# Kernel optimization log

Measured on AMD Instinct MI355X. Metric: run time of the kernel, lower is better.

## Reference

```python
import jax, jax.numpy as jnp
import numpy as np
import math

HEADS = 16
DIMS = 1024
SEQ_LEN = 2048
RANK_K = 128
BATCH = 8


def setup_inputs() -> dict:
    key = jax.random.key(0)
    ks = jax.random.split(key, 14)
    dh_std = 1.0 / math.sqrt(DIMS)
    proj_std = 1.0 / math.sqrt(RANK_K)
    inp = {
        "q": jax.random.normal(ks[0], (BATCH, SEQ_LEN, DIMS), jnp.float32),
        "k": jax.random.normal(ks[1], (BATCH, SEQ_LEN, DIMS), jnp.float32),
        "v": jax.random.normal(ks[2], (BATCH, SEQ_LEN, DIMS), jnp.float32),
        # nn.Linear weights [out, in], bias [out]
        "Wq": jax.random.uniform(ks[3], (DIMS, DIMS), jnp.float32, -dh_std, dh_std),
        "bq": jax.random.uniform(ks[4], (DIMS,), jnp.float32, -dh_std, dh_std),
        "Wk": jax.random.uniform(ks[5], (DIMS, DIMS), jnp.float32, -dh_std, dh_std),
        "bk": jax.random.uniform(ks[6], (DIMS,), jnp.float32, -dh_std, dh_std),
        "Wv": jax.random.uniform(ks[7], (DIMS, DIMS), jnp.float32, -dh_std, dh_std),
        "bv": jax.random.uniform(ks[8], (DIMS,), jnp.float32, -dh_std, dh_std),
        # Linformer low-rank projections [seq_length, k], uniform(-1/sqrt(k), 1/sqrt(k))
        "proj_k": jax.random.uniform(ks[9], (SEQ_LEN, RANK_K), jnp.float32, -proj_std, proj_std),
        "proj_v": jax.random.uniform(ks[10], (SEQ_LEN, RANK_K), jnp.float32, -proj_std, proj_std),
        "Wo": jax.random.uniform(ks[11], (DIMS, DIMS), jnp.float32, -dh_std, dh_std),
        "bo": jax.random.uniform(ks[12], (DIMS,), jnp.float32, -dh_std, dh_std),
    }
    return inp


def reference(q, k, v, Wq, bq, Wk, bk, Wv, bv, proj_k, proj_v, Wo, bo):
    B, N, D = q.shape
    H = HEADS
    dh = D // H
    Kr = proj_k.shape[1]

    kp = k @ Wk.T + bk                       # [B, N, D]
    # faithful to original: plain reshape (view), NOT a head-split transpose
    qp = (q @ Wq.T + bq).reshape(B, H, N, dh)  # [B, H, N, dh]
    vp = v @ Wv.T + bv                       # [B, N, D]

    pk = jnp.einsum('bnd,nk->bkd', kp, proj_k[:N])  # [B, Kr, D]
    pv = jnp.einsum('bnd,nk->bkd', vp, proj_v[:N])  # [B, Kr, D]
    pk = pk.reshape(B, Kr, H, dh).transpose(0, 2, 1, 3)  # [B, H, Kr, dh]
    pv = pv.reshape(B, Kr, H, dh).transpose(0, 2, 1, 3)  # [B, H, Kr, dh]

    # scores [B,H,N,Kr] -> transposed to [B,H,Kr,N]; softmax over N (seq) axis
    scores = jnp.einsum('bhnd,bhkd->bhkn', qp, pk) / math.sqrt(dh)
    attn = jax.nn.softmax(scores, axis=-1)   # [B, H, Kr, N]
    out = jnp.einsum('bhkn,bhkd->bhnd', attn, pv)  # [B, H, N, dh]
    out = out.transpose(0, 2, 1, 3).reshape(B, N, D)
    return out @ Wo.T + bo
```

## Files before the change

### kernel.cpp

```cpp
#include <hip/hip_runtime.h>

typedef unsigned short u16;
typedef unsigned int   u32;
typedef __attribute__((ext_vector_type(4))) float fx4;
typedef __attribute__((ext_vector_type(8))) __bf16 bf16x8;
typedef __attribute__((ext_vector_type(8))) unsigned short us8;
typedef __attribute__((ext_vector_type(2))) unsigned int u32x2;

__device__ __forceinline__ u16 f2bf(float x){
  u32 u = __builtin_bit_cast(u32, x);
  u += 0x7fffu + ((u >> 16) & 1u);
  return (u16)(u >> 16);
}
__device__ __forceinline__ float b2f(u16 h){
  u32 u = ((u32)h) << 16;
  return __builtin_bit_cast(float, u);
}
__device__ __forceinline__ void gld16(const void* g, void* l){
  __builtin_amdgcn_global_load_lds(
      (const __attribute__((address_space(1))) u32*)g,
      (__attribute__((address_space(3))) u32*)l, 16, 0, 0);
}
__device__ __forceinline__ void xcd_remap(u32& bx, u32& by, u32& bz){
  u32 nx = gridDim.x, ny = gridDim.y, nz = gridDim.z;
  u32 nwg = nx * ny * nz;
  u32 orig = (blockIdx.z * ny + blockIdx.y) * nx + blockIdx.x;
  u32 lid = (orig & 7u) * (nwg >> 3) + (orig >> 3);
  bx = lid % nx;
  u32 rem = lid / nx;
  by = rem % ny;
  bz = rem / ny;
}

__global__ __launch_bounds__(256) void k_f2bfAll(const float* __restrict__ w0,
                                                 const float* __restrict__ w1,
                                                 const float* __restrict__ w2,
                                                 const float* __restrict__ w3,
                                                 const float* __restrict__ q,
                                                 u16* __restrict__ wout,
                                                 u16* __restrict__ qout,
                                                 float* __restrict__ zbuf){
  if (blockIdx.x == 0 && blockIdx.y == 0) zbuf[threadIdx.x] = 0.f;
  const int y = blockIdx.y;
  const float* src;
  u16* dst;
  if (y < 4){
    src = y == 0 ? w0 : y == 1 ? w1 : y == 2 ? w2 : w3;
    dst = wout + (long)y * 1048576;
  } else {
    src = q + (long)(y - 4) * 1048576;
    dst = qout + (long)(y - 4) * 1048576;
  }
  int i = blockIdx.x * 256 + threadIdx.x;
  const int stride = gridDim.x * 256;
  for (; i < 131072; i += stride){
    const float4* p = (const float4*)src + (long)i * 2;
    float4 a = p[0], b = p[1];
    us8 o = { f2bf(a.x), f2bf(a.y), f2bf(a.z), f2bf(a.w),
              f2bf(b.x), f2bf(b.y), f2bf(b.z), f2bf(b.w) };
    *((us8*)dst + i) = o;
  }
}

__global__ __launch_bounds__(256) void k_tconvKV(const float* __restrict__ ksrc,
                                                 const float* __restrict__ vsrc,
                                                 u16* __restrict__ kT){
  const int z = blockIdx.z;
  const float* in = (z >= 8 ? vsrc : ksrc) + (long)(z & 7) * 2097152;
  u16* out = kT + (long)(z >> 3) * 16777216 + (long)(z & 7) * 2097152;
  const int c0 = blockIdx.x * 64, r0 = blockIdx.y * 64;
  const int t = threadIdx.x;
  const int c4 = t & 15, r4 = t >> 4;
  float4 f[4];
  #pragma unroll
  for (int i = 0; i < 4; ++i)
    f[i] = *(const float4*)(in + (long)(r0 + r4 * 4 + i) * 1024 + c0 + c4 * 4);
  #pragma unroll
  for (int j = 0; j < 4; ++j){
    u32 lo = (u32)f2bf(((const float*)&f[0])[j]) | ((u32)f2bf(((const float*)&f[1])[j]) << 16);
    u32 hi = (u32)f2bf(((const float*)&f[2])[j]) | ((u32)f2bf(((const float*)&f[3])[j]) << 16);
    u32x2 pr = { lo, hi };
    *(u32x2*)(out + (long)(c0 + c4 * 4 + j) * 2048 + r0 + r4 * 4) = pr;
  }
}

__global__ __launch_bounds__(256) void k_tconvP(const float* __restrict__ pjk,
                                                const float* __restrict__ pjv,
                                                u16* __restrict__ projT,
                                                float* __restrict__ ssum){
  const int z = blockIdx.z;
  const float* in = z ? pjv : pjk;
  u16* out = projT + z * 262144;
  float* colsum = ssum + z * 128;
  const int c0 = blockIdx.x * 64, r0 = blockIdx.y * 64;
  __shared__ u16 tile[64][66];
  __shared__ float red[256];
  const int t = threadIdx.x;
  const int cc = t & 63, wq = t >> 6;
  float part = 0.f;
  #pragma unroll
  for (int i = 0; i < 16; ++i){
    int rr = i * 4 + wq;
    float v = in[(long)(r0 + rr) * 128 + c0 + cc];
    tile[rr][cc] = f2bf(v);
    part += v;
  }
  red[t] = part;
  __syncthreads();
  if (t < 64){
    float s = red[t] + red[t + 64] + red[t + 128] + red[t + 192];
    atomicAdd(&colsum[c0 + t], s);
  }
  __syncthreads();
  const int oc0 = t >> 5, jb = (t & 31) * 2;
  #pragma unroll
  for (int i = 0; i < 8; ++i){
    int oc = oc0 + i * 8;
    u32 pk2 = (u32)tile[jb][oc] | ((u32)tile[jb + 1][oc] << 16);
    *(u32*)(out + (long)(c0 + oc) * 2048 + r0 + jb) = pk2;
  }
}

template<int BM, int BN, int MODE, int EPI, typename OutT>
__global__ __launch_bounds__(256) void k_gemm(
    const u16* __restrict__ A, int lda, long sAz,
    const u16* __restrict__ B, int ldb, long sBz,
    OutT* __restrict__ C, int ldc, long sCz,
    int K, const float* __restrict__ bias, const float* __restrict__ srow, float scale)
{
  constexpr int BK = 64;
  constexpr int FM = BM / 32, FN = BN / 32;
  __shared__ u16 ldsA[BM * BK];
  __shared__ u16 ldsB[BN * BK];
  u32 bx, by, bz;
  xcd_remap(bx, by, bz);
  const long z = bz;
  if constexpr (MODE == 0){ A += z * sAz; B += z * sBz; C += z * sCz; }
  if constexpr (MODE == 3){ long p = z >> 3, bb = z & 7;
                            A += p * 262144; B += p * 16777216 + bb * 2097152;
                            C += p * 1048576 + bb * 131072; }
  const int t = threadIdx.x;
  const int lane = t & 63;
  const int w = t >> 6, wm = w >> 1, wn = w & 1;
  const int r15 = lane & 15, g = lane >> 4;
  const int m0 = by * BM, n0 = bx * BN;
  fx4 acc[FM][FN] = {};
  constexpr int CA = BM * BK / (8 * 256);
  constexpr int CB = BN * BK / (8 * 256);
  for (int kt = 0; kt < K; kt += BK){
    #pragma unroll
    for (int i = 0; i < CA; ++i){
      int ch = i * 256 + t, row = ch >> 3, cc = ch & 7;
      gld16(A + (long)(m0 + row) * lda + kt + cc * 8, (char*)ldsA + ch * 16);
    }
    #pragma unroll
    for (int i = 0; i < CB; ++i){
      int ch = i * 256 + t, row = ch >> 3, cc = ch & 7;
      gld16(B + (long)(n0 + row) * ldb + kt + cc * 8, (char*)ldsB + ch * 16);
    }
    __syncthreads();
    #pragma unroll
    for (int ks = 0; ks < 2; ++ks){
      bf16x8 af[FM], bfv[FN];
      #pragma unroll
      for (int mf = 0; mf < FM; ++mf)
        af[mf] = *(const bf16x8*)&ldsA[(wm * (BM/2) + mf * 16 + r15) * BK + ks * 32 + g * 8];
      #pragma unroll
      for (int nf = 0; nf < FN; ++nf)
        bfv[nf] = *(const bf16x8*)&ldsB[(wn * (BN/2) + nf * 16 + r15) * BK + ks * 32 + g * 8];
      #pragma unroll
      for (int mf = 0; mf < FM; ++mf)
        #pragma unroll
        for (int nf = 0; nf < FN; ++nf)
          acc[mf][nf] = __builtin_amdgcn_mfma_f32_16x16x32_bf16(af[mf], bfv[nf], acc[mf][nf], 0, 0, 0);
    }
    __syncthreads();
  }
  #pragma unroll
  for (int mf = 0; mf < FM; ++mf){
    #pragma unroll
    for (int nf = 0; nf < FN; ++nf){
      const int row0 = m0 + wm * (BM/2) + mf * 16 + g * 4;
      const int col  = n0 + wn * (BN/2) + nf * 16 + r15;
      float vv[4];
      #pragma unroll
      for (int r = 0; r < 4; ++r){
        float v = acc[mf][nf][r];
        if constexpr (EPI == 1) v += bias[col];
        vv[r] = v;
      }
      #pragma unroll
      for (int r = 0; r < 4; ++r){
        if constexpr (sizeof(OutT) == 2) C[(long)(row0 + r) * ldc + col] = (OutT)f2bf(vv[r]);
        else                             C[(long)(row0 + r) * ldc + col] = (OutT)vv[r];
      }
    }
  }
}

__global__ __launch_bounds__(256) void k_pkpv(
    const u16* __restrict__ ck, const u16* __restrict__ Wk_bf,
    const u16* __restrict__ Wv_bf, const float* __restrict__ bk,
    const float* __restrict__ bv, const float* __restrict__ ssum,
    u16* __restrict__ pk, u16* __restrict__ pvT)
{
  constexpr int BM = 64, BN = 64, BK = 64;
  __shared__ u16 ldsA[BM * BK];
  __shared__ u16 ldsB[BN * BK];
  u32 bx, by, bz;
  xcd_remap(bx, by, bz);
  const int half = bz >> 3, b = bz & 7;
  const u16* A = ck + half * 1048576 + b * 131072;
  const u16* B = half ? Wv_bf : Wk_bf;
  const float* bias = half ? bv : bk;
  const float* srow = ssum + half * 128;
  const float scale = half ? 1.f : 0.125f;
  const int t = threadIdx.x;
  const int lane = t & 63;
  const int w = t >> 6, wm = w >> 1, wn = w & 1;
  const int r15 = lane & 15, g = lane >> 4;
  const int m0 = by * BM, n0 = bx * BN;
  fx4 acc[2][2] = {};
  for (int kt = 0; kt < 1024; kt += BK){
    #pragma unroll
    for (int i = 0; i < 2; ++i){
      int ch = i * 256 + t, row = ch >> 3, cc = ch & 7;
      gld16(A + (long)(m0 + row) * 1024 + kt + cc * 8, (char*)ldsA + ch * 16);
    }
    #pragma unroll
    for (int i = 0; i < 2; ++i){
      int ch = i * 256 + t, row = ch >> 3, cc = ch & 7;
      gld16(B + (long)(n0 + row) * 1024 + kt + cc * 8, (char*)ldsB + ch * 16);
    }
    __syncthreads();
    #pragma unroll
    for (int ks = 0; ks < 2; ++ks){
      bf16x8 af[2], bfv[2];
      #pragma unroll
      for (int mf = 0; mf < 2; ++mf)
        af[mf] = *(const bf16x8*)&ldsA[(wm * 32 + mf * 16 + r15) * BK + ks * 32 + g * 8];
      #pragma unroll
      for (int nf = 0; nf < 2; ++nf)
        bfv[nf] = *(const bf16x8*)&ldsB[(wn * 32 + nf * 16 + r15) * BK + ks * 32 + g * 8];
      #pragma unroll
      for (int mf = 0; mf < 2; ++mf)
        #pragma unroll
        for (int nf = 0; nf < 2; ++nf)
          acc[mf][nf] = __builtin_amdgcn_mfma_f32_16x16x32_bf16(af[mf], bfv[nf], acc[mf][nf], 0, 0, 0);
    }
    __syncthreads();
  }
  #pragma unroll
  for (int mf = 0; mf < 2; ++mf){
    #pragma unroll
    for (int nf = 0; nf < 2; ++nf){
      const int row0 = m0 + wm * 32 + mf * 16 + g * 4;
      const int col  = n0 + wn * 32 + nf * 16 + r15;
      float vv[4];
      #pragma unroll
      for (int r = 0; r < 4; ++r)
        vv[r] = (acc[mf][nf][r] + srow[row0 + r] * bias[col]) * scale;
      if (!half){
        #pragma unroll
        for (int r = 0; r < 4; ++r)
          pk[b * 131072 + (long)(row0 + r) * 1024 + col] = f2bf(vv[r]);
      } else {
        u32 lo = (u32)f2bf(vv[0]) | ((u32)f2bf(vv[1]) << 16);
        u32 hi = (u32)f2bf(vv[2]) | ((u32)f2bf(vv[3]) << 16);
        u32x2 pk2 = { lo, hi };
        *(u32x2*)(pvT + b * 131072 + (long)col * 128 + row0) = pk2;
      }
    }
  }
}

template<int EPI, typename OutT>
__global__ __launch_bounds__(512, 1) void k_gemm256b(
    const u16* __restrict__ A, int lda,
    const u16* __restrict__ B, int ldb,
    OutT* __restrict__ C, int ldc,
    int K, const float* __restrict__ bias)
{
  constexpr int BM = 256, BN = 256, BK = 64;
  __shared__ u16 ldsA[2][BM * BK];
  __shared__ u16 ldsB[2][BN * BK];
  u32 bx, by, bz;
  xcd_remap(bx, by, bz);
  const int m0 = by * BM, n0 = bx * BN;
  const int t = threadIdx.x, lane = t & 63, w = t >> 6;
  const int wm = w >> 2, wn = w & 3;
  const int r15 = lane & 15, g = lane >> 4;
  const int NT = K >> 6;

  auto stA = [&](int buf, int half, int kt){
    #pragma unroll
    for (int j = 0; j < 2; ++j){
      int ch = j * 512 + t, row = ch >> 3, cc = ch & 7;
      gld16(A + (long)(m0 + half * 128 + row) * lda + kt + ((cc ^ (row & 7)) * 8),
            (char*)ldsA[buf] + half * 16384 + ch * 16);
    }
  };
  auto stB = [&](int buf, int half, int kt){
    #pragma unroll
    for (int j = 0; j < 2; ++j){
      int ch = j * 512 + t, row = ch >> 3, cc = ch & 7;
      gld16(B + (long)(n0 + half * 128 + row) * ldb + kt + ((cc ^ (row & 7)) * 8),
            (char*)ldsB[buf] + half * 16384 + ch * 16);
    }
  };

  stB(0,0,0); stB(0,1,0); stA(0,0,0); stA(0,1,0);
  if (NT > 1){ stB(1,0,BK); stB(1,1,BK); stA(1,0,BK); }
  asm volatile("s_waitcnt vmcnt(6)" ::: "memory");
  __builtin_amdgcn_s_barrier();
  asm volatile("" ::: "memory");

  fx4 acc[8][4] = {};
  for (int tt = 0; tt < NT; ++tt){
    const int buf = tt & 1;
    bf16x8 a[2][4], b01[2][2], b23[2][2];
    #pragma unroll
    for (int ks = 0; ks < 2; ++ks)
      #pragma unroll
      for (int mf = 0; mf < 4; ++mf){
        int row = wm * 128 + mf * 16 + r15;
        a[ks][mf] = *(const bf16x8*)((const char*)ldsA[buf] + row * 128 + (((ks*4+g) ^ (r15 & 7)) * 16));
      }
    #pragma unroll
    for (int ks = 0; ks < 2; ++ks)
      #pragma unroll
      for (int nf = 0; nf < 2; ++nf){
        int row = wn * 64 + nf * 16 + r15;
        b01[ks][nf] = *(const bf16x8*)((const char*)ldsB[buf] + row * 128 + (((ks*4+g) ^ (r15 & 7)) * 16));
      }
    if (tt + 1 < NT) stA(buf ^ 1, 1, (tt + 1) * BK);
    __builtin_amdgcn_s_setprio(1);
    #pragma unroll
    for (int ks = 0; ks < 2; ++ks)
      #pragma unroll
      for (int mf = 0; mf < 4; ++mf)
        #pragma unroll
        for (int nf = 0; nf < 2; ++nf)
          acc[mf][nf] = __builtin_amdgcn_mfma_f32_16x16x32_bf16(a[ks][mf], b01[ks][nf], acc[mf][nf], 0, 0, 0);
    __builtin_amdgcn_s_setprio(0);
    asm volatile("" ::: "memory");
    __builtin_amdgcn_s_barrier();
    asm volatile("" ::: "memory");
    #pragma unroll
    for (int ks = 0; ks < 2; ++ks)
      #pragma unroll
      for (int nf = 0; nf < 2; ++nf){
        int row = wn * 64 + (nf + 2) * 16 + r15;
        b23[ks][nf] = *(const bf16x8*)((const char*)ldsB[buf] + row * 128 + (((ks*4+g) ^ (r15 & 7)) * 16));
      }
    __builtin_amdgcn_s_setprio(1);
    #pragma unroll
    for (int ks = 0; ks < 2; ++ks)
      #pragma unroll
      for (int mf = 0; mf < 4; ++mf)
        #pragma unroll
        for (int nf = 0; nf < 2; ++nf)
          acc[mf][nf + 2] = __builtin_amdgcn_mfma_f32_16x16x32_bf16(a[ks][mf], b23[ks][nf], acc[mf][nf + 2], 0, 0, 0);
    __builtin_amdgcn_s_setprio(0);
    asm volatile("" ::: "memory");
    __builtin_amdgcn_s_barrier();
    asm volatile("" ::: "memory");
    #pragma unroll
    for (int ks = 0; ks < 2; ++ks)
      #pragma unroll
      for (int mf = 0; mf < 4; ++mf){
        int row = wm * 128 + (mf + 4) * 16 + r15;
        a[ks][mf] = *(const bf16x8*)((const char*)ldsA[buf] + row * 128 + (((ks*4+g) ^ (r15 & 7)) * 16));
      }
    if (tt + 2 < NT) stB(buf, 0, (tt + 2) * BK);
    __builtin_amdgcn_s_setprio(1);
    #pragma unroll
    for (int ks = 0; ks < 2; ++ks)
      #pragma unroll
      for (int mf = 0; mf < 4; ++mf)
        #pragma unroll
        for (int nf = 0; nf < 2; ++nf)
          acc[mf + 4][nf + 2] = __builtin_amdgcn_mfma_f32_16x16x32_bf16(a[ks][mf], b23[ks][nf], acc[mf + 4][nf + 2], 0, 0, 0);
    __builtin_amdgcn_s_setprio(0);
    asm volatile("" ::: "memory");
    __builtin_amdgcn_s_barrier();
    asm volatile("" ::: "memory");
    if (tt + 2 < NT){ stA(buf, 0, (tt + 2) * BK); stB(buf, 1, (tt + 2) * BK); }
    __builtin_amdgcn_s_setprio(1);
    #pragma unroll
    for (int ks = 0; ks < 2; ++ks)
      #pragma unroll
      for (int mf = 0; mf < 4; ++mf)
        #pragma unroll
        for (int nf = 0; nf < 2; ++nf)
          acc[mf + 4][nf] = __builtin_amdgcn_mfma_f32_16x16x32_bf16(a[ks][mf], b01[ks][nf], acc[mf + 4][nf], 0, 0, 0);
    __builtin_amdgcn_s_setprio(0);
    if (tt + 2 < NT)      { asm volatile("s_waitcnt vmcnt(6)" ::: "memory"); }
    else if (tt + 1 < NT) { asm volatile("s_waitcnt vmcnt(0)" ::: "memory"); }
    asm volatile("" ::: "memory");
    __builtin_amdgcn_s_barrier();
    asm volatile("" ::: "memory");
  }

  #pragma unroll
  for (int mf = 0; mf < 8; ++mf)
    #pragma unroll
    for (int nf = 0; nf < 4; ++nf){
      const int row0 = m0 + wm * 128 + mf * 16 + g * 4;
      const int col  = n0 + wn * 64 + nf * 16 + r15;
      float bcol = 0.f;
      if constexpr (EPI == 1) bcol = bias[col];
      #pragma unroll
      for (int r = 0; r < 4; ++r){
        float vv = acc[mf][nf][r] + bcol;
        if constexpr (sizeof(OutT) == 2) C[(long)(row0 + r) * ldc + col] = (OutT)f2bf(vv);
        else                             C[(long)(row0 + r) * ldc + col] = (OutT)vv;
      }
    }
}

__global__ __launch_bounds__(512) void k_stats(const u16* __restrict__ pk,
                                               const u16* __restrict__ qp,
                                               float* __restrict__ zpart){
  const int hf = blockIdx.x, z = blockIdx.y;
  const int b = z >> 4, h = z & 15;
  const u16* pkh = pk + b * 131072 + h * 64;
  const u16* qph = qp + (long)z * 131072;
  __shared__ u16 pkL[128 * 64];
  __shared__ float zred[8][128];
  const int t = threadIdx.x, lane = t & 63, w = t >> 6;
  const int r15 = lane & 15, g = lane >> 4;
  #pragma unroll
  for (int i = 0; i < 2; ++i){
    int ch = i * 512 + t, row = ch >> 3, cc = ch & 7;
    int csrc = cc ^ (row & 7);
    gld16(pkh + (long)row * 1024 + csrc * 8, (char*)pkL + ch * 16);
  }
  __syncthreads();
  float zacc[8][4] = {};
  for (int c = 0; c < 4; ++c){
    const int n0 = hf * 1024 + w * 128 + c * 32;
    fx4 acc[8][2] = {};
    #pragma unroll
    for (int ks = 0; ks < 2; ++ks){
      bf16x8 bq[2];
      #pragma unroll
      for (int nf = 0; nf < 2; ++nf)
        bq[nf] = *(const bf16x8*)(qph + (long)(n0 + nf * 16 + r15) * 64 + ks * 32 + g * 8);
      #pragma unroll
      for (int mf = 0; mf < 8; ++mf){
        int row = mf * 16 + r15;
        int x = (ks * 4 + g) ^ (row & 7);
        bf16x8 a = *(const bf16x8*)((const char*)pkL + row * 128 + x * 16);
        #pragma unroll
        for (int nf = 0; nf < 2; ++nf)
          acc[mf][nf] = __builtin_amdgcn_mfma_f32_16x16x32_bf16(a, bq[nf], acc[mf][nf], 0, 0, 0);
      }
    }
    #pragma unroll
    for (int mf = 0; mf < 8; ++mf)
      #pragma unroll
      for (int nf = 0; nf < 2; ++nf)
        #pragma unroll
        for (int r = 0; r < 4; ++r)
          zacc[mf][r] += __expf(acc[mf][nf][r]);
  }
  #pragma unroll
  for (int mf = 0; mf < 8; ++mf)
    #pragma unroll
    for (int r = 0; r < 4; ++r){
      float v = zacc[mf][r];
      v += __shfl_xor(v, 1); v += __shfl_xor(v, 2);
      v += __shfl_xor(v, 4); v += __shfl_xor(v, 8);
      zacc[mf][r] = v;
    }
  if (r15 == 0){
    #pragma unroll
    for (int mf = 0; mf < 8; ++mf)
      #pragma unroll
      for (int r = 0; r < 4; ++r)
        zred[w][mf * 16 + g * 4 + r] = zacc[mf][r];
  }
  __syncthreads();
  if (t < 128){
    float s = 0.f;
    #pragma unroll
    for (int w2 = 0; w2 < 8; ++w2) s += zred[w2][t];
    zpart[hf * 16384 + (long)z * 128 + t] = s;
  }
}

__global__ __launch_bounds__(256) void k_attn(const u16* __restrict__ pk,
                                              const u16* __restrict__ qp,
                                              const u16* __restrict__ pvT,
                                              const float* __restrict__ zpart,
                                              u16* __restrict__ outh){
  u32 bx, by, bz;
  xcd_remap(bx, by, bz);
  const int z = by, nb = bx;
  const int b = z >> 4, h = z & 15;
  const u16* pkh = pk  + b * 131072 + h * 64;
  const u16* qph = qp  + (long)z * 131072;
  const u16* pvh = pvT + b * 131072 + h * 8192;
  __shared__ u16 pkL[128 * 64];
  __shared__ u16 ptL[4][32 * 132];
  __shared__ float zL[128];
  const int t = threadIdx.x, lane = t & 63, w = t >> 6;
  const int r15 = lane & 15, g = lane >> 4;
  #pragma unroll
  for (int i = 0; i < 4; ++i){
    int ch = i * 256 + t, row = ch >> 3, cc = ch & 7;
    int csrc = cc ^ (row & 7);
    gld16(pkh + (long)row * 1024 + csrc * 8, (char*)pkL + ch * 16);
  }
  if (t < 128)
    zL[t] = 1.0f / (zpart[(long)z * 128 + t] + zpart[16384 + (long)z * 128 + t]);
  __syncthreads();
  const int n0 = nb * 128 + w * 32;
  fx4 acc[8][2] = {};
  #pragma unroll
  for (int ks = 0; ks < 2; ++ks){
    bf16x8 bq[2];
    #pragma unroll
    for (int nf = 0; nf < 2; ++nf)
      bq[nf] = *(const bf16x8*)(qph + (long)(n0 + nf * 16 + r15) * 64 + ks * 32 + g * 8);
    #pragma unroll
    for (int mf = 0; mf < 8; ++mf){
      int row = mf * 16 + r15;
      int x = (ks * 4 + g) ^ (row & 7);
      bf16x8 a = *(const bf16x8*)((const char*)pkL + row * 128 + x * 16);
      #pragma unroll
      for (int nf = 0; nf < 2; ++nf)
        acc[mf][nf] = __builtin_amdgcn_mfma_f32_16x16x32_bf16(a, bq[nf], acc[mf][nf], 0, 0, 0);
    }
  }
  u16* pt = ptL[w];
  #pragma unroll
  for (int mf = 0; mf < 8; ++mf){
    const int kb = mf * 16 + g * 4;
    const float z0 = zL[kb], z1 = zL[kb + 1], z2 = zL[kb + 2], z3 = zL[kb + 3];
    #pragma unroll
    for (int nf = 0; nf < 2; ++nf){
      const int nl = nf * 16 + r15;
      u32 lo = (u32)f2bf(__expf(acc[mf][nf][0]) * z0) |
               ((u32)f2bf(__expf(acc[mf][nf][1]) * z1) << 16);
      u32 hi = (u32)f2bf(__expf(acc[mf][nf][2]) * z2) |
               ((u32)f2bf(__expf(acc[mf][nf][3]) * z3) << 16);
      u32x2 pkd = { lo, hi };
      *(u32x2*)(pt + nl * 132 + kb) = pkd;
    }
  }
  fx4 o[2][4] = {};
  #pragma unroll
  for (int ks = 0; ks < 4; ++ks){
    bf16x8 bv[4];
    #pragma unroll
    for (int nf = 0; nf < 4; ++nf)
      bv[nf] = *(const bf16x8*)(pvh + (long)(nf * 16 + r15) * 128 + ks * 32 + g * 8);
    #pragma unroll
    for (int mf = 0; mf < 2; ++mf){
      bf16x8 pa = *(const bf16x8*)(pt + (mf * 16 + r15) * 132 + ks * 32 + g * 8);
      #pragma unroll
      for (int nf = 0; nf < 4; ++nf)
        o[mf][nf] = __builtin_amdgcn_mfma_f32_16x16x32_bf16(pa, bv[nf], o[mf][nf], 0, 0, 0);
    }
  }
  u16* og = outh + ((long)b * 2048 + n0) * 1024 + h * 64;
  #pragma unroll
  for (int mf = 0; mf < 2; ++mf)
    #pragma unroll
    for (int nf = 0; nf < 4; ++nf)
      #pragma unroll
      for (int r = 0; r < 4; ++r){
        int nl = mf * 16 + g * 4 + r;
        og[(long)nl * 1024 + nf * 16 + r15] = f2bf(o[mf][nf][r]);
      }
}

extern "C" void kernel_launch(void* const* d_in, const int* in_sizes, int n_in,
                              void* d_out, int out_size, void* d_ws, size_t ws_size,
                              hipStream_t stream)
{
  const float* q   = (const float*)d_in[0];
  const float* k   = (const float*)d_in[1];
  const float* v   = (const float*)d_in[2];
  const float* Wq  = (const float*)d_in[3];
  const float* bq  = (const float*)d_in[4];
  const float* Wk  = (const float*)d_in[5];
  const float* bk  = (const float*)d_in[6];
  const float* Wv  = (const float*)d_in[7];
  const float* bv  = (const float*)d_in[8];
  const float* pjk = (const float*)d_in[9];
  const float* pjv = (const float*)d_in[10];
  const float* Wo  = (const float*)d_in[11];
  const float* bo  = (const float*)d_in[12];

  if (ws_size < 152044544u) return;

  char* ws = (char*)d_ws;
  u16*  q_bf  = (u16*)(ws + 0);
  u16*  kT    = (u16*)(ws + 33554432);
  u16*  vT    = (u16*)(ws + 67108864);
  u16*  W_bf  = (u16*)(ws + 100663296);
  u16*  projT = (u16*)(ws + 109051904);
  float* sk   = (float*)(ws + 110100480);
  u16*  qp    = (u16*)(ws + 110101504);
  u16*  ck    = (u16*)(ws + 143655936);
  u16*  pk    = (u16*)(ws + 147850240);
  u16*  pvT   = (u16*)(ws + 149947392);
  float* zpart = (float*)(ws + 33554432);
  u16*  outh  = (u16*)(ws + 0);
  u16*  Wq_bf = W_bf, *Wk_bf = W_bf + 1048576, *Wv_bf = W_bf + 2097152, *Wo_bf = W_bf + 3145728;

  k_f2bfAll<<<dim3(128,20), 256, 0, stream>>>(Wq, Wk, Wv, Wo, q, W_bf, q_bf, sk);
  k_tconvP<<<dim3(2,32,2), 256, 0, stream>>>(pjk, pjv, projT, sk);
  k_tconvKV<<<dim3(16,32,16), 256, 0, stream>>>(k, v, kT);

  k_gemm256b<1,u16><<<dim3(4,64), 512, 0, stream>>>(
      q_bf,1024, Wq_bf,1024, qp,1024, 1024, bq);
  k_gemm<128,64,3,0,u16><<<dim3(16,1,16), 256, 0, stream>>>(
      projT,2048,0, kT,2048,0, ck,1024,0, 2048, nullptr, nullptr, 1.f);
  k_pkpv<<<dim3(16,2,16), 256, 0, stream>>>(ck, Wk_bf, Wv_bf, bk, bv, sk, pk, pvT);
  k_stats<<<dim3(2,128), 512, 0, stream>>>(pk, qp, zpart);
  k_attn<<<dim3(16,128), 256, 0, stream>>>(pk, qp, pvT, zpart, outh);
  k_gemm256b<1,float><<<dim3(4,64), 512, 0, stream>>>(
      outh,1024, Wo_bf,1024, (float*)d_out,1024, 1024, bo);
}
```

Measured before the change: 267.4 us.

## Fuse K/V transpose-convert into projection GEMM with triple-buffered LDS pipeline

```diff
diff --git a/kernel.cpp b/kernel.cpp
--- a/kernel.cpp
+++ b/kernel.cpp
@@ -4,6 +4,7 @@
 typedef unsigned int   u32;
 typedef __attribute__((ext_vector_type(4))) float fx4;
 typedef __attribute__((ext_vector_type(8))) __bf16 bf16x8;
+typedef __attribute__((ext_vector_type(4))) __bf16 bf16x4;
 typedef __attribute__((ext_vector_type(8))) unsigned short us8;
 typedef __attribute__((ext_vector_type(2))) unsigned int u32x2;
 
@@ -62,28 +63,6 @@
   }
 }
 
-__global__ __launch_bounds__(256) void k_tconvKV(const float* __restrict__ ksrc,
-                                                 const float* __restrict__ vsrc,
-                                                 u16* __restrict__ kT){
-  const int z = blockIdx.z;
-  const float* in = (z >= 8 ? vsrc : ksrc) + (long)(z & 7) * 2097152;
-  u16* out = kT + (long)(z >> 3) * 16777216 + (long)(z & 7) * 2097152;
-  const int c0 = blockIdx.x * 64, r0 = blockIdx.y * 64;
-  const int t = threadIdx.x;
-  const int c4 = t & 15, r4 = t >> 4;
-  float4 f[4];
-  #pragma unroll
-  for (int i = 0; i < 4; ++i)
-    f[i] = *(const float4*)(in + (long)(r0 + r4 * 4 + i) * 1024 + c0 + c4 * 4);
-  #pragma unroll
-  for (int j = 0; j < 4; ++j){
-    u32 lo = (u32)f2bf(((const float*)&f[0])[j]) | ((u32)f2bf(((const float*)&f[1])[j]) << 16);
-    u32 hi = (u32)f2bf(((const float*)&f[2])[j]) | ((u32)f2bf(((const float*)&f[3])[j]) << 16);
-    u32x2 pr = { lo, hi };
-    *(u32x2*)(out + (long)(c0 + c4 * 4 + j) * 2048 + r0 + r4 * 4) = pr;
-  }
-}
-
 __global__ __launch_bounds__(256) void k_tconvP(const float* __restrict__ pjk,
                                                 const float* __restrict__ pjv,
                                                 u16* __restrict__ projT,
@@ -121,81 +100,123 @@
   }
 }
 
-template<int BM, int BN, int MODE, int EPI, typename OutT>
-__global__ __launch_bounds__(256) void k_gemm(
-    const u16* __restrict__ A, int lda, long sAz,
-    const u16* __restrict__ B, int ldb, long sBz,
-    OutT* __restrict__ C, int ldc, long sCz,
-    int K, const float* __restrict__ bias, const float* __restrict__ srow, float scale)
+__global__ __launch_bounds__(256) void k_gemmTN(
+    const u16* __restrict__ projT, const float* __restrict__ ksrc,
+    const float* __restrict__ vsrc, u16* __restrict__ ck)
 {
-  constexpr int BK = 64;
-  constexpr int FM = BM / 32, FN = BN / 32;
-  __shared__ u16 ldsA[BM * BK];
-  __shared__ u16 ldsB[BN * BK];
-  u32 bx, by, bz;
-  xcd_remap(bx, by, bz);
-  const long z = bz;
-  if constexpr (MODE == 0){ A += z * sAz; B += z * sBz; C += z * sCz; }
-  if constexpr (MODE == 3){ long p = z >> 3, bb = z & 7;
-                            A += p * 262144; B += p * 16777216 + bb * 2097152;
-                            C += p * 1048576 + bb * 131072; }
-  const int t = threadIdx.x;
-  const int lane = t & 63;
-  const int w = t >> 6, wm = w >> 1, wn = w & 1;
+  u32 bx, by, bz; xcd_remap(bx, by, bz);
+  const int p = bz >> 3, b = bz & 7;
+  const u16* A = projT + p * 262144 + by * 64 * 2048;
+  const float* S = (p ? vsrc : ksrc) + (long)b * 2097152;
+  u16* C = ck + p * 1048576 + b * 131072 + by * 65536;
+  const int d0 = bx * 64;
+  __shared__ u16 ldsA[3][64 * 64];
+  __shared__ u16 ldsB[3][64 * 72];
+  const int t = threadIdx.x, lane = t & 63, w = t >> 6;
+  const int wm = w >> 1, wn = w & 1;
   const int r15 = lane & 15, g = lane >> 4;
-  const int m0 = by * BM, n0 = bx * BN;
-  fx4 acc[FM][FN] = {};
-  constexpr int CA = BM * BK / (8 * 256);
-  constexpr int CB = BN * BK / (8 * 256);
-  for (int kt = 0; kt < K; kt += BK){
-    #pragma unroll
-    for (int i = 0; i < CA; ++i){
+  const int c4 = t & 15, r4 = t >> 4;
+
+  auto ldA = [&](int kt, int buf){
+    #pragma unroll
+    for (int i = 0; i < 2; ++i){
       int ch = i * 256 + t, row = ch >> 3, cc = ch & 7;
-      gld16(A + (long)(m0 + row) * lda + kt + cc * 8, (char*)ldsA + ch * 16);
-    }
-    #pragma unroll
-    for (int i = 0; i < CB; ++i){
-      int ch = i * 256 + t, row = ch >> 3, cc = ch & 7;
-      gld16(B + (long)(n0 + row) * ldb + kt + cc * 8, (char*)ldsB + ch * 16);
-    }
-    __syncthreads();
+      gld16(A + (long)row * 2048 + kt + ((cc ^ (row & 7)) * 8),
+            (char*)ldsA[buf] + ch * 16);
+    }
+  };
+  auto ldS = [&](int kt, float4* f){
+    #pragma unroll
+    for (int i = 0; i < 4; ++i)
+      f[i] = *(const float4*)(S + (long)(kt + r4 * 4 + i) * 1024 + d0 + c4 * 4);
+  };
+  auto wrB = [&](const float4* f, int buf){
+    #pragma unroll
+    for (int j = 0; j < 4; ++j){
+      const int d = c4 * 4 + j;
+      u32 lo = (u32)f2bf(((const float*)&f[0])[j]) | ((u32)f2bf(((const float*)&f[1])[j]) << 16);
+      u32 hi = (u32)f2bf(((const float*)&f[2])[j]) | ((u32)f2bf(((const float*)&f[3])[j]) << 16);
+      u32x2 pr = { lo, hi };
+      *(u32x2*)&ldsB[buf][d * 72 + ((r4 ^ (d & 15)) * 4)] = pr;
+    }
+  };
+
+  fx4 acc[2][2] = {};
+  auto compute = [&](int buf){
     #pragma unroll
     for (int ks = 0; ks < 2; ++ks){
-      bf16x8 af[FM], bfv[FN];
-      #pragma unroll
-      for (int mf = 0; mf < FM; ++mf)
-        af[mf] = *(const bf16x8*)&ldsA[(wm * (BM/2) + mf * 16 + r15) * BK + ks * 32 + g * 8];
-      #pragma unroll
-      for (int nf = 0; nf < FN; ++nf)
-        bfv[nf] = *(const bf16x8*)&ldsB[(wn * (BN/2) + nf * 16 + r15) * BK + ks * 32 + g * 8];
-      #pragma unroll
-      for (int mf = 0; mf < FM; ++mf)
-        #pragma unroll
-        for (int nf = 0; nf < FN; ++nf)
+      bf16x8 af[2], bfv[2];
+      #pragma unroll
+      for (int mf = 0; mf < 2; ++mf){
+        int row = wm * 32 + mf * 16 + r15;
+        af[mf] = *(const bf16x8*)((const char*)ldsA[buf] + row * 128 +
+                                  (((ks * 4 + g) ^ (row & 7)) * 16));
+      }
+      #pragma unroll
+      for (int nf = 0; nf < 2; ++nf){
+        const int d = wn * 32 + nf * 16 + r15, x = d & 15;
+        const int q0 = ks * 8 + g * 2;
+        bf16x4 lo = *(const bf16x4*)&ldsB[buf][d * 72 + ((q0 ^ x) * 4)];
+        bf16x4 hi = *(const bf16x4*)&ldsB[buf][d * 72 + (((q0 + 1) ^ x) * 4)];
+        bfv[nf] = __builtin_shufflevector(lo, hi, 0, 1, 2, 3, 4, 5, 6, 7);
+      }
+      #pragma unroll
+      for (int mf = 0; mf < 2; ++mf)
+        #pragma unroll
+        for (int nf = 0; nf < 2; ++nf)
           acc[mf][nf] = __builtin_amdgcn_mfma_f32_16x16x32_bf16(af[mf], bfv[nf], acc[mf][nf], 0, 0, 0);
     }
-    __syncthreads();
-  }
-  #pragma unroll
-  for (int mf = 0; mf < FM; ++mf){
-    #pragma unroll
-    for (int nf = 0; nf < FN; ++nf){
-      const int row0 = m0 + wm * (BM/2) + mf * 16 + g * 4;
-      const int col  = n0 + wn * (BN/2) + nf * 16 + r15;
-      float vv[4];
-      #pragma unroll
-      for (int r = 0; r < 4; ++r){
-        float v = acc[mf][nf][r];
-        if constexpr (EPI == 1) v += bias[col];
-        vv[r] = v;
-      }
-      #pragma unroll
-      for (int r = 0; r < 4; ++r){
-        if constexpr (sizeof(OutT) == 2) C[(long)(row0 + r) * ldc + col] = (OutT)f2bf(vv[r]);
-        else                             C[(long)(row0 + r) * ldc + col] = (OutT)vv[r];
-      }
-    }
-  }
+  };
+
+  float4 fa[4], fb[4];
+  ldS(0, fa); ldA(0, 0);
+  ldS(64, fb); ldA(64, 1);
+  asm volatile("s_waitcnt vmcnt(6)" ::: "memory");
+  wrB(fa, 0);
+  asm volatile("s_waitcnt lgkmcnt(0)" ::: "memory");
+  __builtin_amdgcn_s_barrier();
+  asm volatile("" ::: "memory");
+
+  for (int tt = 0; tt < 32; tt += 2){
+    {
+      const bool pf = (tt + 2 < 32);
+      if (pf){ ldS((tt + 2) * 64, fa); ldA((tt + 2) * 64, (tt + 2) % 3); }
+      asm volatile("" ::: "memory");
+      compute(tt % 3);
+      if (pf) { asm volatile("s_waitcnt vmcnt(6)" ::: "memory"); }
+      else    { asm volatile("s_waitcnt vmcnt(0)" ::: "memory"); }
+      wrB(fb, (tt + 1) % 3);
+      asm volatile("s_waitcnt lgkmcnt(0)" ::: "memory");
+      __builtin_amdgcn_s_barrier();
+      asm volatile("" ::: "memory");
+    }
+    {
+      const bool pf = (tt + 3 < 32);
+      const bool hv = (tt + 2 < 32);
+      if (pf){ ldS((tt + 3) * 64, fb); ldA((tt + 3) * 64, (tt + 3) % 3); }
+      asm volatile("" ::: "memory");
+      compute((tt + 1) % 3);
+      if (hv){
+        if (pf) { asm volatile("s_waitcnt vmcnt(6)" ::: "memory"); }
+        else    { asm volatile("s_waitcnt vmcnt(0)" ::: "memory"); }
+        wrB(fa, (tt + 2) % 3);
+      }
+      asm volatile("s_waitcnt lgkmcnt(0)" ::: "memory");
+      __builtin_amdgcn_s_barrier();
+      asm volatile("" ::: "memory");
+    }
+  }
+
+  #pragma unroll
+  for (int mf = 0; mf < 2; ++mf)
+    #pragma unroll
+    for (int nf = 0; nf < 2; ++nf){
+      const int row0 = wm * 32 + mf * 16 + g * 4;
+      const int col  = d0 + wn * 32 + nf * 16 + r15;
+      #pragma unroll
+      for (int r = 0; r < 4; ++r)
+        C[(long)(row0 + r) * 1024 + col] = f2bf(acc[mf][nf][r]);
+    }
 }
 
 __global__ __launch_bounds__(256) void k_pkpv(
@@ -599,8 +620,7 @@
 
   char* ws = (char*)d_ws;
   u16*  q_bf  = (u16*)(ws + 0);
-  u16*  kT    = (u16*)(ws + 33554432);
-  u16*  vT    = (u16*)(ws + 67108864);
+  float* zpart = (float*)(ws + 33554432);
   u16*  W_bf  = (u16*)(ws + 100663296);
   u16*  projT = (u16*)(ws + 109051904);
   float* sk   = (float*)(ws + 110100480);
@@ -608,18 +628,15 @@
   u16*  ck    = (u16*)(ws + 143655936);
   u16*  pk    = (u16*)(ws + 147850240);
   u16*  pvT   = (u16*)(ws + 149947392);
-  float* zpart = (float*)(ws + 33554432);
   u16*  outh  = (u16*)(ws + 0);
   u16*  Wq_bf = W_bf, *Wk_bf = W_bf + 1048576, *Wv_bf = W_bf + 2097152, *Wo_bf = W_bf + 3145728;
 
   k_f2bfAll<<<dim3(128,20), 256, 0, stream>>>(Wq, Wk, Wv, Wo, q, W_bf, q_bf, sk);
   k_tconvP<<<dim3(2,32,2), 256, 0, stream>>>(pjk, pjv, projT, sk);
-  k_tconvKV<<<dim3(16,32,16), 256, 0, stream>>>(k, v, kT);
 
   k_gemm256b<1,u16><<<dim3(4,64), 512, 0, stream>>>(
       q_bf,1024, Wq_bf,1024, qp,1024, 1024, bq);
-  k_gemm<128,64,3,0,u16><<<dim3(16,1,16), 256, 0, stream>>>(
-      projT,2048,0, kT,2048,0, ck,1024,0, 2048, nullptr, nullptr, 1.f);
+  k_gemmTN<<<dim3(16,2,16), 256, 0, stream>>>(projT, k, v, ck);
   k_pkpv<<<dim3(16,2,16), 256, 0, stream>>>(ck, Wk_bf, Wv_bf, bk, bv, sk, pk, pvT);
   k_stats<<<dim3(2,128), 512, 0, stream>>>(pk, qp, zpart);
   k_attn<<<dim3(16,128), 256, 0, stream>>>(pk, qp, pvT, zpart, outh);
```

After: 221.7 us. 17.1% less time.
